# Kernel optimization log

Measured on AMD Instinct MI355X. Metric: run time of the kernel, lower is better.

## Reference

```python
import jax, jax.numpy as jnp
import numpy as np

N_NODES = 50000
N_EDGES = 1600000
IN_DIM = 128
HID = 128
N_GRAPHS = 64
N_CLASSES = 1


def _seg_sum(x, ids, n):
    return jax.ops.segment_sum(x, ids, num_segments=n)


def _gcn_layer(h, W, b, src, dst, src_isqrt, dst_isqrt):
    # DGL GraphConv, norm='both': D_dst^{-1/2} A D_src^{-1/2} (h W) + b
    hw = h @ W                                  # [N, out]
    msg = (hw * src_isqrt[:, None])[src]        # gather -> [E, out]
    agg = _seg_sum(msg, dst, h.shape[0])        # scatter-add -> [N, out]
    return agg * dst_isqrt[:, None] + b


def setup_inputs() -> dict:
    key = jax.random.key(0)
    ks = jax.random.split(key, 16)
    x = jax.random.normal(ks[0], (N_NODES, IN_DIM), dtype=jnp.float32)
    src = jax.random.randint(ks[1], (N_EDGES,), 0, N_NODES)
    dst = jax.random.randint(ks[2], (N_EDGES,), 0, N_NODES)
    graph_id = jnp.sort(jax.random.randint(ks[3], (N_NODES,), 0, N_GRAPHS))
    s = 1.0 / np.sqrt(HID)
    params = {
        'W1': jax.random.uniform(ks[4], (IN_DIM, HID), jnp.float32, -s, s),
        'b1': jnp.zeros((HID,), jnp.float32),
        'W2': jax.random.uniform(ks[5], (HID, HID), jnp.float32, -s, s),
        'b2': jnp.zeros((HID,), jnp.float32),
        'Wc1': jax.random.uniform(ks[6], (HID, HID // 2), jnp.float32, -s, s),
        'bc1': jnp.zeros((HID // 2,), jnp.float32),
        'Wc2': jax.random.uniform(ks[7], (HID // 2, HID // 4), jnp.float32, -s, s),
        'bc2': jnp.zeros((HID // 4,), jnp.float32),
        'Wc3': jax.random.uniform(ks[8], (HID // 4, HID // 8), jnp.float32, -s, s),
        'bc3': jnp.zeros((HID // 8,), jnp.float32),
        'Wc4': jax.random.uniform(ks[9], (HID // 8, N_CLASSES), jnp.float32, -s, s),
        'bc4': jnp.zeros((N_CLASSES,), jnp.float32),
    }
    return dict(x=x, src=src, dst=dst, graph_id=graph_id, num_graphs=N_GRAPHS, **params)


def reference(x, src, dst, graph_id, num_graphs, W1, b1, W2, b2,
              Wc1, bc1, Wc2, bc2, Wc3, bc3, Wc4, bc4):
    n = x.shape[0]
    ones = jnp.ones((src.shape[0],), x.dtype)
    out_deg = jnp.clip(_seg_sum(ones, src, n), 1.0)
    in_deg = jnp.clip(_seg_sum(ones, dst, n), 1.0)
    src_isqrt = jax.lax.rsqrt(out_deg)
    dst_isqrt = jax.lax.rsqrt(in_deg)

    h = jax.nn.relu(_gcn_layer(x, W1, b1, src, dst, src_isqrt, dst_isqrt))
    h = jax.nn.relu(_gcn_layer(h, W2, b2, src, dst, src_isqrt, dst_isqrt))

    # dgl.mean_nodes: per-graph mean of node features
    sums = _seg_sum(h, graph_id, num_graphs)                       # [G, HID]
    cnts = jnp.clip(_seg_sum(jnp.ones((n,), h.dtype), graph_id, num_graphs), 1.0)
    hg = sums / cnts[:, None]

    o = jax.nn.relu(hg @ Wc1 + bc1)
    o = jax.nn.relu(o @ Wc2 + bc2)
    o = jax.nn.relu(o @ Wc3 + bc3)
    return o @ Wc4 + bc4
```

## Files before the change

kernel.cpp:

```cpp
#include <hip/hip_runtime.h>
#include <hip/hip_fp16.h>

#define FDIM 128
#define NGRAPH 64
#define CBLK 256
#define OCH2 12800
#define OSL 64
#define FSTAGE 12288

typedef _Float16 f16;
typedef f16 f16x8 __attribute__((ext_vector_type(8)));
typedef float f32x4 __attribute__((ext_vector_type(4)));
typedef float f32x2 __attribute__((ext_vector_type(2)));

__device__ __forceinline__ int lower_bound_i(const int* a, int n, int v) {
    int lo = 0, hi = n;
    while (lo < hi) { int m = (lo + hi) >> 1; if (a[m] < v) lo = m + 1; else hi = m; }
    return lo;
}

__global__ __launch_bounds__(256) void k_pre(
        const float* __restrict__ W1, f16* __restrict__ W1h, f16* __restrict__ W1l,
        const float* __restrict__ W2, f16* __restrict__ W2h, f16* __restrict__ W2l,
        float* __restrict__ hg, const int* __restrict__ src, const int* __restrict__ dst,
        unsigned* __restrict__ od_part, int* __restrict__ partial,
        int E, int NBIN, int CE4, int NH) {
    __shared__ __align__(16) unsigned shmem_u[OCH2];
    const int t = threadIdx.x;
    int b = blockIdx.x;
    if (b < 128) {
        int i = b * 256 + t;
        if (i < NGRAPH * FDIM) hg[i] = 0.f;
        int j = i & 16383;
        int k = j >> 7, n = j & 127;
        const float* W = (i < 16384) ? W1 : W2;
        f16* Wh = (i < 16384) ? W1h : W2h;
        f16* Wl = (i < 16384) ? W1l : W2l;
        float v = W[j];
        f16 hi = (f16)v;
        Wh[n * FDIM + k] = hi;
        Wl[n * FDIM + k] = (f16)(v - (float)hi);
    } else if (b < 128 + CBLK) {
        b -= 128;
        int* lds = (int*)shmem_u;
        for (int i = t; i < 4 * 257; i += 256) lds[i] = 0;
        __syncthreads();
        const int wv = t >> 6;
        int* hh = &lds[wv * 257];
        const int s = b * CE4, e = min(E, s + CE4);
        for (int i = s + t * 4; i < e; i += 1024) {
            if (i + 4 <= e) {
                uint4 d4 = *(const uint4*)&dst[i];
                atomicAdd(&hh[d4.x >> 8], 1);
                atomicAdd(&hh[d4.y >> 8], 1);
                atomicAdd(&hh[d4.z >> 8], 1);
                atomicAdd(&hh[d4.w >> 8], 1);
            } else {
                for (int j = i; j < e; j++) atomicAdd(&hh[dst[j] >> 8], 1);
            }
        }
        __syncthreads();
        for (int i = t; i < NBIN; i += 256)
            partial[i * CBLK + b] = lds[i] + lds[257 + i] + lds[514 + i] + lds[771 + i];
    } else {
        const int ob = b - 128 - CBLK;
        const int c  = ob >> 6;
        const int sl = ob & (OSL - 1);
        for (int i = t; i < OCH2; i += 256) shmem_u[i] = 0u;
        __syncthreads();
        const int plo = c * OCH2;
        const int vlo = plo * 2;
        const int SE = (((E + OSL - 1) / OSL) + 3) & ~3;
        const int s = sl * SE, e = min(E, s + SE);
        for (int i = s + t * 4; i < e; i += 1024) {
            if (i + 4 <= e) {
                uint4 s4 = *(const uint4*)&src[i];
                int v0 = (int)s4.x - vlo, v1 = (int)s4.y - vlo;
                int v2 = (int)s4.z - vlo, v3 = (int)s4.w - vlo;
                if ((unsigned)v0 < (unsigned)(2 * OCH2))
                    atomicAdd(&shmem_u[v0 >> 1], 1u << ((v0 & 1) * 16));
                if ((unsigned)v1 < (unsigned)(2 * OCH2))
                    atomicAdd(&shmem_u[v1 >> 1], 1u << ((v1 & 1) * 16));
                if ((unsigned)v2 < (unsigned)(2 * OCH2))
                    atomicAdd(&shmem_u[v2 >> 1], 1u << ((v2 & 1) * 16));
                if ((unsigned)v3 < (unsigned)(2 * OCH2))
                    atomicAdd(&shmem_u[v3 >> 1], 1u << ((v3 & 1) * 16));
            } else {
                for (int j = i; j < e; j++) {
                    int v = src[j] - vlo;
                    if ((unsigned)v < (unsigned)(2 * OCH2))
                        atomicAdd(&shmem_u[v >> 1], 1u << ((v & 1) * 16));
                }
            }
        }
        __syncthreads();
        const int hiN = min(NH - plo, OCH2);
        for (int i = t; i < hiN; i += 256)
            od_part[(size_t)sl * NH + plo + i] = shmem_u[i];
    }
}

__global__ __launch_bounds__(256) void k_scan(
        const int* __restrict__ partial, int* __restrict__ offs, int* __restrict__ bsum,
        int M, const unsigned* __restrict__ od_part, float* __restrict__ sisq,
        int NH, int N, int NBIN) {
    __shared__ int lds[256];
    const int t = threadIdx.x;
    int b = blockIdx.x;
    if (b < NBIN) {
        int i = b * 256 + t;
        int v = (i < M) ? partial[i] : 0;
        lds[t] = v;
        __syncthreads();
        for (int off = 1; off < 256; off <<= 1) {
            int x = (t >= off) ? lds[t - off] : 0;
            __syncthreads();
            lds[t] += x;
            __syncthreads();
        }
        if (i < M) offs[i] = lds[t] - v;
        if (t == 255) bsum[b] = lds[t];
    } else {
        b -= NBIN;
        const int i = b * 256 + t;
        if (i < NH) {
            unsigned lo = 0, hi = 0;
#pragma unroll 8
            for (int s = 0; s < OSL; s++) {
                unsigned v = od_part[(size_t)s * NH + i];
                lo += v & 0xFFFFu;
                hi += v >> 16;
            }
            const int n0 = 2 * i, n1 = 2 * i + 1;
            sisq[n0] = rsqrtf((float)max((int)lo, 1));
            if (n1 < N) sisq[n1] = rsqrtf((float)max((int)hi, 1));
        }
    }
}

__global__ __launch_bounds__(256) void k_coarse_scatter(
        const int* __restrict__ src, const int* __restrict__ dst,
        const int* __restrict__ offs, const int* __restrict__ bsum,
        const int* __restrict__ partial,
        unsigned* __restrict__ coarse_buf, int E, int CE4, int NBIN) {
    __shared__ int G[256], lo[256], cur[256], sc[256];
    __shared__ unsigned stage[6272];
    const int t = threadIdx.x, b = blockIdx.x;
    int v = (t < NBIN) ? bsum[t] : 0;
    sc[t] = v;
    __syncthreads();
    for (int off = 1; off < 256; off <<= 1) {
        int x = (t >= off) ? sc[t - off] : 0;
        __syncthreads();
        sc[t] += x;
        __syncthreads();
    }
    if (t < NBIN) G[t] = offs[t * CBLK + b] + (sc[t] - v);
    __syncthreads();
    int hv = (t < NBIN) ? partial[t * CBLK + b] : 0;
    sc[t] = hv;
    __syncthreads();
    for (int off = 1; off < 256; off <<= 1) {
        int x = (t >= off) ? sc[t - off] : 0;
        __syncthreads();
        sc[t] += x;
        __syncthreads();
    }
    lo[t] = sc[t] - hv;
    cur[t] = sc[t] - hv;
    __syncthreads();
    const int s = b * CE4, e = min(E, s + CE4);
    for (int i = s + t * 4; i < e; i += 1024) {
        if (i + 4 <= e) {
            uint4 d4 = *(const uint4*)&dst[i];
            uint4 s4 = *(const uint4*)&src[i];
            int p0 = atomicAdd(&cur[d4.x >> 8], 1);
            int p1 = atomicAdd(&cur[d4.y >> 8], 1);
            int p2 = atomicAdd(&cur[d4.z >> 8], 1);
            int p3 = atomicAdd(&cur[d4.w >> 8], 1);
            stage[p0] = (d4.x << 16) | s4.x;
            stage[p1] = (d4.y << 16) | s4.y;
            stage[p2] = (d4.z << 16) | s4.z;
            stage[p3] = (d4.w << 16) | s4.w;
        } else {
            for (int j = i; j < e; j++) {
                unsigned d = (unsigned)dst[j];
                int p = atomicAdd(&cur[d >> 8], 1);
                stage[p] = (d << 16) | (unsigned)src[j];
            }
        }
    }
    __syncthreads();
    const int nloc = e - s;
    for (int i = t; i < nloc; i += 256) {
        unsigned p = stage[i];
        int f = p >> 24;
        coarse_buf[G[f] + (i - lo[f])] = p;
    }
}

template<bool IN_F16>
__device__ __forceinline__ void gemm_body(
        f16* smem, float* sisql, int blk,
        const void* __restrict__ Xv, const f16* __restrict__ Wh,
        const f16* __restrict__ Wl, const float* __restrict__ sisq,
        unsigned char* __restrict__ out, int N) {
    const int t = threadIdx.x;
    const int w = t >> 6;
    const int lane = t & 63;
    const int base = blk * 128;

    if (t < 128) {
        int row = base + t;
        sisql[t] = (row < N) ? sisq[row] : 1.f;
    }
    for (int i = t; i < 2048; i += 256) {
        int n = i >> 4, kc = (i & 15) * 8;
        *(uint4*)&smem[n * 136 + kc] = *(const uint4*)&Wh[n * FDIM + kc];
    }
    __syncthreads();

    const int mrow = lane & 15;
    const int kq = (lane >> 4) * 8;
    const int arow0 = min(base + w * 32 + mrow, N - 1);
    const int arow1 = min(base + w * 32 + 16 + mrow, N - 1);

    f16x8 a0[4], a1[4];
    if (IN_F16) {
        const f16* X = (const f16*)Xv;
#pragma unroll
        for (int kk = 0; kk < 4; kk++) {
            a0[kk] = *(const f16x8*)&X[(size_t)arow0 * FDIM + kk * 32 + kq];
            a1[kk] = *(const f16x8*)&X[(size_t)arow1 * FDIM + kk * 32 + kq];
        }
    } else {
        const float* X = (const float*)Xv;
#pragma unroll
        for (int kk = 0; kk < 4; kk++) {
            float4 u0 = *(const float4*)&X[(size_t)arow0 * FDIM + kk * 32 + kq];
            float4 u1 = *(const float4*)&X[(size_t)arow0 * FDIM + kk * 32 + kq + 4];
            float4 v0 = *(const float4*)&X[(size_t)arow1 * FDIM + kk * 32 + kq];
            float4 v1 = *(const float4*)&X[(size_t)arow1 * FDIM + kk * 32 + kq + 4];
            f16x8 av;
            av[0] = (f16)u0.x; av[1] = (f16)u0.y; av[2] = (f16)u0.z; av[3] = (f16)u0.w;
            av[4] = (f16)u1.x; av[5] = (f16)u1.y; av[6] = (f16)u1.z; av[7] = (f16)u1.w;
            a0[kk] = av;
            av[0] = (f16)v0.x; av[1] = (f16)v0.y; av[2] = (f16)v0.z; av[3] = (f16)v0.w;
            av[4] = (f16)v1.x; av[5] = (f16)v1.y; av[6] = (f16)v1.z; av[7] = (f16)v1.w;
            a1[kk] = av;
        }
    }

    f32x4 acc0[8], acc1[8];
#pragma unroll
    for (int nt = 0; nt < 8; nt++) {
        acc0[nt] = (f32x4){0.f, 0.f, 0.f, 0.f};
        acc1[nt] = (f32x4){0.f, 0.f, 0.f, 0.f};
    }

#pragma unroll
    for (int kk = 0; kk < 4; kk++) {
#pragma unroll
        for (int nt = 0; nt < 8; nt++) {
            f16x8 bh = *(const f16x8*)&smem[(nt * 16 + mrow) * 136 + kk * 32 + kq];
            f16x8 bl = *(const f16x8*)&Wl[(nt * 16 + mrow) * FDIM + kk * 32 + kq];
            acc0[nt] = __builtin_amdgcn_mfma_f32_16x16x32_f16(a0[kk], bh, acc0[nt], 0, 0, 0);
            acc1[nt] = __builtin_amdgcn_mfma_f32_16x16x32_f16(a1[kk], bh, acc1[nt], 0, 0, 0);
            acc0[nt] = __builtin_amdgcn_mfma_f32_16x16x32_f16(a0[kk], bl, acc0[nt], 0, 0, 0);
            acc1[nt] = __builtin_amdgcn_mfma_f32_16x16x32_f16(a1[kk], bl, acc1[nt], 0, 0, 0);
        }
    }

    const int r0 = (lane >> 4) * 4;
    float sv0[4], sv1[4];
#pragma unroll
    for (int j = 0; j < 4; j++) {
        sv0[j] = sisql[w * 32 + r0 + j];
        sv1[j] = sisql[w * 32 + 16 + r0 + j];
    }
    __syncthreads();
#pragma unroll
    for (int nt = 0; nt < 8; nt++) {
        int c = nt * 16 + mrow;
#pragma unroll
        for (int j = 0; j < 4; j++) {
            smem[(w * 32 + r0 + j) * 136 + c]      = (f16)(acc0[nt][j] * sv0[j]);
            smem[(w * 32 + 16 + r0 + j) * 136 + c] = (f16)(acc1[nt][j] * sv1[j]);
        }
    }
    __syncthreads();
    {
        int r = t >> 1, cb = (t & 1) * 64;
        int row = base + r;
        if (row < N) {
            unsigned char* dstp = out + (size_t)row * FDIM + cb;
#pragma unroll
            for (int g2 = 0; g2 < 4; g2++) {
                unsigned wv[4];
#pragma unroll
                for (int k2 = 0; k2 < 4; k2++) {
                    const f16* p = &smem[r * 136 + cb + g2 * 16 + k2 * 4];
                    int w0 = __builtin_amdgcn_cvt_pk_fp8_f32((float)p[0], (float)p[1], 0, false);
                    w0 = __builtin_amdgcn_cvt_pk_fp8_f32((float)p[2], (float)p[3], w0, true);
                    wv[k2] = (unsigned)w0;
                }
                uint4 u;
                u.x = wv[0]; u.y = wv[1]; u.z = wv[2]; u.w = wv[3];
                *(uint4*)&dstp[g2 * 16] = u;
            }
        }
    }
}

__global__ __launch_bounds__(256) void k_fine_gemm(
        const unsigned* __restrict__ coarse_buf, const int* __restrict__ bsum,
        unsigned short* __restrict__ csr_src, int* __restrict__ row_ptr,
        int N, int E, int NBIN,
        const float* __restrict__ x, const f16* __restrict__ Wh,
        const f16* __restrict__ Wl, const float* __restrict__ sisq,
        unsigned char* __restrict__ hws) {
    __shared__ __align__(16) f16 smem[128 * 136];
    __shared__ float sisql[128];
    const int t = threadIdx.x;
    const int g = blockIdx.x;
    if (g >= NBIN) {
        gemm_body<false>(smem, sisql, g - NBIN, x, Wh, Wl, sisq, hws, N);
        return;
    }
    int* h   = (int*)smem;
    int* sc  = h + 256;
    int* cur = h + 512;
    int* lo  = h + 768;
    unsigned short* stage = (unsigned short*)(h + 1024);
    int bv = (t < NBIN) ? bsum[t] : 0;
    sc[t] = bv;
    __syncthreads();
    for (int off = 1; off < 256; off <<= 1) {
        int xx = (t >= off) ? sc[t - off] : 0;
        __syncthreads();
        sc[t] += xx;
        __syncthreads();
    }
    if (t == 0) { cur[0] = sc[g] - bsum[g]; cur[1] = sc[g]; }
    __syncthreads();
    const int s = cur[0], e = cur[1];
    __syncthreads();
    h[t] = 0;
    __syncthreads();
    for (int i = s + t; i < e; i += 256)
        atomicAdd(&h[(coarse_buf[i] >> 16) & 255], 1);
    __syncthreads();
    int v = h[t];
    sc[t] = v;
    __syncthreads();
    for (int off = 1; off < 256; off <<= 1) {
        int xx = (t >= off) ? sc[t - off] : 0;
        __syncthreads();
        sc[t] += xx;
        __syncthreads();
    }
    const int excl = sc[t] - v;
    const int node = g * 256 + t;
    if (node < N) row_ptr[node] = s + excl;
    if (node == N) row_ptr[N] = s + excl;
    lo[t] = excl;
    cur[t] = excl;
    __syncthreads();
    const int len = e - s;
    if (len <= FSTAGE) {
        for (int i = s + t; i < e; i += 256) {
            unsigned p = coarse_buf[i];
            int f = (p >> 16) & 255;
            int pos = atomicAdd(&cur[f], 1);
            stage[pos] = (unsigned short)(p & 0xFFFFu);
        }
        __syncthreads();
        for (int i = t; i < len; i += 256)
            csr_src[s + i] = stage[i];
    } else {
        for (int i = s + t; i < e; i += 256) {
            unsigned p = coarse_buf[i];
            int f = (p >> 16) & 255;
            int pos = atomicAdd(&cur[f], 1);
            csr_src[s + pos] = (unsigned short)(p & 0xFFFFu);
        }
    }
    if (g == NBIN - 1 && t == 0 && (N & 255) == 0) row_ptr[N] = E;
}

__global__ __launch_bounds__(256) void k_gemm2(
        const f16* __restrict__ X, const f16* __restrict__ Wh,
        const f16* __restrict__ Wl, const float* __restrict__ sisq,
        unsigned char* __restrict__ out, int N) {
    __shared__ __align__(16) f16 smem[128 * 136];
    __shared__ float sisql[128];
    gemm_body<true>(smem, sisql, blockIdx.x, X, Wh, Wl, sisq, out, N);
}

__device__ __forceinline__ void accF8(float* acc, uint2 v) {
    f32x2 a0 = __builtin_amdgcn_cvt_pk_f32_fp8((int)v.x, false);
    f32x2 a1 = __builtin_amdgcn_cvt_pk_f32_fp8((int)v.x, true);
    f32x2 a2 = __builtin_amdgcn_cvt_pk_f32_fp8((int)v.y, false);
    f32x2 a3 = __builtin_amdgcn_cvt_pk_f32_fp8((int)v.y, true);
    acc[0] += a0.x; acc[1] += a0.y; acc[2] += a1.x; acc[3] += a1.y;
    acc[4] += a2.x; acc[5] += a2.y; acc[6] += a3.x; acc[7] += a3.y;
}

template<bool POOL>
__global__ __launch_bounds__(256) void k_aggregate(
        const unsigned char* __restrict__ hws,
        const unsigned short* __restrict__ csr_src,
        const int* __restrict__ row_ptr,
        const float* __restrict__ bias, f16* __restrict__ out,
        const int* __restrict__ gid, float* __restrict__ hg, int N) {
    const int t = threadIdx.x;
    const int node = blockIdx.x * 8 + (t >> 5);
    const int ln = t & 31;
    const int half = ln >> 4;
    const int fbase = (ln & 15) * 8;

    int s = 0, e = 0;
    if (node < N) { s = row_ptr[node]; e = row_ptr[node + 1]; }
    const int len = e - s;
    const int mid = s + ((len + 1) >> 1);
    int i  = half ? mid : s;
    const int en = half ? e : mid;

    float acc[8];
#pragma unroll
    for (int j = 0; j < 8; j++) acc[j] = 0.f;

    for (; i + 8 <= en; i += 8) {
        int u[8];
#pragma unroll
        for (int j = 0; j < 8; j++) u[j] = csr_src[i + j];
        uint2 v[8];
#pragma unroll
        for (int j = 0; j < 8; j++)
            v[j] = *(const uint2*)(hws + (size_t)u[j] * FDIM + fbase);
#pragma unroll
        for (int j = 0; j < 8; j++) accF8(acc, v[j]);
    }
    if (i + 4 <= en) {
        int u[4];
#pragma unroll
        for (int j = 0; j < 4; j++) u[j] = csr_src[i + j];
        uint2 v[4];
#pragma unroll
        for (int j = 0; j < 4; j++)
            v[j] = *(const uint2*)(hws + (size_t)u[j] * FDIM + fbase);
#pragma unroll
        for (int j = 0; j < 4; j++) accF8(acc, v[j]);
        i += 4;
    }
    for (; i < en; i++) {
        int u = csr_src[i];
        uint2 v = *(const uint2*)(hws + (size_t)u * FDIM + fbase);
        accF8(acc, v);
    }

#pragma unroll
    for (int j = 0; j < 8; j++) acc[j] += __shfl_xor(acc[j], 16, 64);

    const float d = rsqrtf((float)max(len, 1));
    float res[8];
#pragma unroll
    for (int j = 0; j < 8; j++)
        res[j] = fmaxf(fmaf(acc[j], d, bias[fbase + j]), 0.f);

    if (!POOL) {
        if (node < N && half == 0) {
            f16 r16[8];
#pragma unroll
            for (int j = 0; j < 8; j++) r16[j] = (f16)res[j];
            *(uint4*)(out + (size_t)node * FDIM + fbase) = *(const uint4*)r16;
        }
    } else {
        __shared__ float hgl[8 * 128];
        const int nfirst = blockIdx.x * 8;
        const int nlast = min(nfirst + 7, N - 1);
        const int g0 = gid[nfirst];
        const int span = gid[nlast] - g0 + 1;
        if (span <= 8) {
            for (int k = t; k < span * 128; k += 256) hgl[k] = 0.f;
            __syncthreads();
            if (node < N && half == 0) {
                const int gg = gid[node] - g0;
#pragma unroll
                for (int j = 0; j < 8; j++)
                    atomicAdd(&hgl[gg * 128 + fbase + j], res[j]);
            }
            __syncthreads();
            for (int k = t; k < span * 128; k += 256)
                atomicAdd(&hg[g0 * 128 + k], hgl[k]);
        } else {
            if (node < N && half == 0) {
                const int gg = gid[node];
#pragma unroll
                for (int j = 0; j < 8; j++)
                    atomicAdd(&hg[gg * 128 + fbase + j], res[j]);
            }
        }
    }
}

__global__ __launch_bounds__(256) void k_mlp(
        const float* __restrict__ hg, const int* __restrict__ gid, int N,
        const float* __restrict__ Wc1, const float* __restrict__ bc1,
        const float* __restrict__ Wc2, const float* __restrict__ bc2,
        const float* __restrict__ Wc3, const float* __restrict__ bc3,
        const float* __restrict__ Wc4, const float* __restrict__ bc4,
        float* __restrict__ out) {
    __shared__ float A[NGRAPH * 128];
    __shared__ float O1[NGRAPH * 64];
    __shared__ float O2[NGRAPH * 32];
    __shared__ float O3[NGRAPH * 16];
    __shared__ float inv_cnt[NGRAPH];
    const int t = threadIdx.x;

    if (t < NGRAPH) {
        int s = lower_bound_i(gid, N, t);
        int e = lower_bound_i(gid, N, t + 1);
        inv_cnt[t] = 1.f / fmaxf((float)(e - s), 1.f);
    }
    __syncthreads();

    for (int i = t; i < NGRAPH * 128; i += 256) A[i] = hg[i] * inv_cnt[i >> 7];
    __syncthreads();

    for (int i = t; i < NGRAPH * 64; i += 256) {
        int g = i >> 6, o = i & 63;
        float a = bc1[o];
        for (int k = 0; k < 128; k++) a = fmaf(A[g * 128 + k], Wc1[k * 64 + o], a);
        O1[i] = fmaxf(a, 0.f);
    }
    __syncthreads();

    for (int i = t; i < NGRAPH * 32; i += 256) {
        int g = i >> 5, o = i & 31;
        float a = bc2[o];
        for (int k = 0; k < 64; k++) a = fmaf(O1[g * 64 + k], Wc2[k * 32 + o], a);
        O2[i] = fmaxf(a, 0.f);
    }
    __syncthreads();

    for (int i = t; i < NGRAPH * 16; i += 256) {
        int g = i >> 4, o = i & 15;
        float a = bc3[o];
        for (int k = 0; k < 32; k++) a = fmaf(O2[g * 32 + k], Wc3[k * 16 + o], a);
        O3[i] = fmaxf(a, 0.f);
    }
    __syncthreads();

    if (t < NGRAPH) {
        float a = bc4[0];
        for (int k = 0; k < 16; k++) a = fmaf(O3[t * 16 + k], Wc4[k], a);
        out[t] = a;
    }
}

extern "C" void kernel_launch(void* const* d_in, const int* in_sizes, int n_in,
                              void* d_out, int out_size, void* d_ws, size_t ws_size,
                              hipStream_t stream) {
    const float* x   = (const float*)d_in[0];
    const int*   src = (const int*)d_in[1];
    const int*   dst = (const int*)d_in[2];
    const int*   gid = (const int*)d_in[3];
    const float* W1  = (const float*)d_in[5];
    const float* b1  = (const float*)d_in[6];
    const float* W2  = (const float*)d_in[7];
    const float* b2  = (const float*)d_in[8];
    const float* Wc1 = (const float*)d_in[9];
    const float* bc1 = (const float*)d_in[10];
    const float* Wc2 = (const float*)d_in[11];
    const float* bc2 = (const float*)d_in[12];
    const float* Wc3 = (const float*)d_in[13];
    const float* bc3 = (const float*)d_in[14];
    const float* Wc4 = (const float*)d_in[15];
    const float* bc4 = (const float*)d_in[16];
    float* out = (float*)d_out;

    const int N = in_sizes[0] / FDIM;
    const int E = in_sizes[1];

    const int NBIN = (N + 255) >> 8;
    const int M    = NBIN * CBLK;
    const int CE4  = (((E + CBLK - 1) / CBLK) + 3) & ~3;
    const int NH   = (N + 1) >> 1;
    const int OC2  = (NH + OCH2 - 1) / OCH2;
    const int MB   = (NH + 255) >> 8;

    char* w = (char*)d_ws;
    size_t off = 0;
    auto alloc = [&](size_t bytes) -> void* {
        void* p = w + off;
        off = (off + bytes + 255) & ~(size_t)255;
        return p;
    };
    unsigned char* hws = (unsigned char*)alloc((size_t)N * FDIM);
    f16*   h       = (f16*)   alloc((size_t)N * FDIM * 2);
    unsigned short* csr_src = (unsigned short*)alloc((size_t)E * 2);
    unsigned* coarse_buf = (unsigned*)alloc((size_t)E * 4);
    unsigned* od_part = (unsigned*)alloc((size_t)OSL * NH * 4);
    int*   partial = (int*)   alloc((size_t)M * 4);
    int*   offs    = (int*)   alloc((size_t)M * 4);
    int*   row_ptr = (int*)   alloc((size_t)(N + 1) * 4);
    float* sisq    = (float*) alloc((size_t)N * 4);
    int*   bsum    = (int*)   alloc(256 * 4);
    float* hg      = (float*) alloc(NGRAPH * FDIM * 4);
    f16*   W1t     = (f16*)   alloc(FDIM * FDIM * 2);
    f16*   W1l     = (f16*)   alloc(FDIM * FDIM * 2);
    f16*   W2t     = (f16*)   alloc(FDIM * FDIM * 2);
    f16*   W2l     = (f16*)   alloc(FDIM * FDIM * 2);

    const int gT = (N + 127) / 128;
    const int gA = (N + 7) / 8;

    k_pre<<<128 + CBLK + OC2 * OSL, 256, 0, stream>>>(
        W1, W1t, W1l, W2, W2t, W2l, hg, src, dst, od_part, partial, E, NBIN, CE4, NH);
    k_scan<<<NBIN + MB, 256, 0, stream>>>(partial, offs, bsum, M, od_part, sisq, NH, N, NBIN);
    k_coarse_scatter<<<CBLK, 256, 0, stream>>>(
        src, dst, offs, bsum, partial, coarse_buf, E, CE4, NBIN);
    k_fine_gemm<<<NBIN + gT, 256, 0, stream>>>(
        coarse_buf, bsum, csr_src, row_ptr, N, E, NBIN,
        x, W1t, W1l, sisq, hws);
    k_aggregate<false><<<gA, 256, 0, stream>>>(hws, csr_src, row_ptr, b1, h, nullptr, nullptr, N);
    k_gemm2<<<gT, 256, 0, stream>>>(h, W2t, W2l, sisq, hws, N);
    k_aggregate<true><<<gA, 256, 0, stream>>>(hws, csr_src, row_ptr, b2, nullptr, gid, hg, N);
    k_mlp<<<1, 256, 0, stream>>>(hg, gid, N, Wc1, bc1, Wc2, bc2, Wc3, bc3, Wc4, bc4, out);
}
```

Measured before the change: 277.6 us.

## Fuse layer-1 aggregation with layer-2 GEMM through shared memory

Merges the first aggregation kernel and the second GEMM into one kernel. Each block gathers and sums neighbor features for 128 nodes into an LDS tile, then runs the MFMA GEMM directly from that tile. This removes the fp16 h buffer round trip through global memory and one launch. In exchange, 128-node blocks do the gather in 8 serial rounds of 16 nodes with one 16-lane group per node, which gives fewer blocks and less latency hiding for the irregular gathers. A separate output buffer avoids overwriting hws while other blocks still read it.

```diff
diff --git a/kernel.cpp b/kernel.cpp
--- a/kernel.cpp
+++ b/kernel.cpp
@@ -388,15 +388,6 @@
     if (g == NBIN - 1 && t == 0 && (N & 255) == 0) row_ptr[N] = E;
 }
 
-__global__ __launch_bounds__(256) void k_gemm2(
-        const f16* __restrict__ X, const f16* __restrict__ Wh,
-        const f16* __restrict__ Wl, const float* __restrict__ sisq,
-        unsigned char* __restrict__ out, int N) {
-    __shared__ __align__(16) f16 smem[128 * 136];
-    __shared__ float sisql[128];
-    gemm_body<true>(smem, sisql, blockIdx.x, X, Wh, Wl, sisq, out, N);
-}
-
 __device__ __forceinline__ void accF8(float* acc, uint2 v) {
     f32x2 a0 = __builtin_amdgcn_cvt_pk_f32_fp8((int)v.x, false);
     f32x2 a1 = __builtin_amdgcn_cvt_pk_f32_fp8((int)v.x, true);
@@ -406,12 +397,148 @@
     acc[4] += a2.x; acc[5] += a2.y; acc[6] += a3.x; acc[7] += a3.y;
 }
 
-template<bool POOL>
-__global__ __launch_bounds__(256) void k_aggregate(
+__global__ __launch_bounds__(256) void k_agg_gemm2(
         const unsigned char* __restrict__ hws,
         const unsigned short* __restrict__ csr_src,
         const int* __restrict__ row_ptr,
-        const float* __restrict__ bias, f16* __restrict__ out,
+        const float* __restrict__ bias,
+        const f16* __restrict__ Wh,
+        const f16* __restrict__ Wl,
+        const float* __restrict__ sisq,
+        unsigned char* __restrict__ out, int N) {
+    __shared__ __align__(16) f16 smem[128 * 136];
+    __shared__ float sisql[128];
+    const int t = threadIdx.x;
+    const int base = blockIdx.x * 128;
+    if (t < 128) {
+        int row = base + t;
+        sisql[t] = (row < N) ? sisq[row] : 1.f;
+    }
+    const int grp = t >> 4;
+    const int l = t & 15;
+    const int fbase = l * 8;
+    for (int k = 0; k < 8; k++) {
+        const int nl = k * 16 + grp;
+        const int node = base + nl;
+        int s = 0, e = 0;
+        if (node < N) { s = row_ptr[node]; e = row_ptr[node + 1]; }
+        float acc[8];
+#pragma unroll
+        for (int j = 0; j < 8; j++) acc[j] = 0.f;
+        int i = s;
+        for (; i + 8 <= e; i += 8) {
+            int u[8];
+#pragma unroll
+            for (int j = 0; j < 8; j++) u[j] = csr_src[i + j];
+            uint2 v[8];
+#pragma unroll
+            for (int j = 0; j < 8; j++)
+                v[j] = *(const uint2*)(hws + (size_t)u[j] * FDIM + fbase);
+#pragma unroll
+            for (int j = 0; j < 8; j++) accF8(acc, v[j]);
+        }
+        if (i + 4 <= e) {
+            int u[4];
+#pragma unroll
+            for (int j = 0; j < 4; j++) u[j] = csr_src[i + j];
+            uint2 v[4];
+#pragma unroll
+            for (int j = 0; j < 4; j++)
+                v[j] = *(const uint2*)(hws + (size_t)u[j] * FDIM + fbase);
+#pragma unroll
+            for (int j = 0; j < 4; j++) accF8(acc, v[j]);
+            i += 4;
+        }
+        for (; i < e; i++) {
+            int u = csr_src[i];
+            uint2 v = *(const uint2*)(hws + (size_t)u * FDIM + fbase);
+            accF8(acc, v);
+        }
+        const float d = rsqrtf((float)max(e - s, 1));
+        f16 r16[8];
+#pragma unroll
+        for (int j = 0; j < 8; j++)
+            r16[j] = (f16)fmaxf(fmaf(acc[j], d, bias[fbase + j]), 0.f);
+        *(uint4*)&smem[nl * 136 + fbase] = *(const uint4*)r16;
+    }
+    __syncthreads();
+
+    const int w = t >> 6;
+    const int lane = t & 63;
+    const int mrow = lane & 15;
+    const int kq = (lane >> 4) * 8;
+    const int ar0 = w * 32 + mrow;
+    const int ar1 = w * 32 + 16 + mrow;
+    f16x8 a0[4], a1[4];
+#pragma unroll
+    for (int kk = 0; kk < 4; kk++) {
+        a0[kk] = *(const f16x8*)&smem[ar0 * 136 + kk * 32 + kq];
+        a1[kk] = *(const f16x8*)&smem[ar1 * 136 + kk * 32 + kq];
+    }
+    f32x4 acc0[8], acc1[8];
+#pragma unroll
+    for (int nt = 0; nt < 8; nt++) {
+        acc0[nt] = (f32x4){0.f, 0.f, 0.f, 0.f};
+        acc1[nt] = (f32x4){0.f, 0.f, 0.f, 0.f};
+    }
+#pragma unroll
+    for (int kk = 0; kk < 4; kk++) {
+#pragma unroll
+        for (int nt = 0; nt < 8; nt++) {
+            f16x8 bh = *(const f16x8*)&Wh[(nt * 16 + mrow) * FDIM + kk * 32 + kq];
+            f16x8 bl = *(const f16x8*)&Wl[(nt * 16 + mrow) * FDIM + kk * 32 + kq];
+            acc0[nt] = __builtin_amdgcn_mfma_f32_16x16x32_f16(a0[kk], bh, acc0[nt], 0, 0, 0);
+            acc1[nt] = __builtin_amdgcn_mfma_f32_16x16x32_f16(a1[kk], bh, acc1[nt], 0, 0, 0);
+            acc0[nt] = __builtin_amdgcn_mfma_f32_16x16x32_f16(a0[kk], bl, acc0[nt], 0, 0, 0);
+            acc1[nt] = __builtin_amdgcn_mfma_f32_16x16x32_f16(a1[kk], bl, acc1[nt], 0, 0, 0);
+        }
+    }
+    const int r0 = (lane >> 4) * 4;
+    float sv0[4], sv1[4];
+#pragma unroll
+    for (int j = 0; j < 4; j++) {
+        sv0[j] = sisql[w * 32 + r0 + j];
+        sv1[j] = sisql[w * 32 + 16 + r0 + j];
+    }
+    __syncthreads();
+#pragma unroll
+    for (int nt = 0; nt < 8; nt++) {
+        int c = nt * 16 + mrow;
+#pragma unroll
+        for (int j = 0; j < 4; j++) {
+            smem[(w * 32 + r0 + j) * 136 + c]      = (f16)(acc0[nt][j] * sv0[j]);
+            smem[(w * 32 + 16 + r0 + j) * 136 + c] = (f16)(acc1[nt][j] * sv1[j]);
+        }
+    }
+    __syncthreads();
+    {
+        int r = t >> 1, cb = (t & 1) * 64;
+        int row = base + r;
+        if (row < N) {
+            unsigned char* dstp = out + (size_t)row * FDIM + cb;
+#pragma unroll
+            for (int g2 = 0; g2 < 4; g2++) {
+                unsigned wv[4];
+#pragma unroll
+                for (int k2 = 0; k2 < 4; k2++) {
+                    const f16* p = &smem[r * 136 + cb + g2 * 16 + k2 * 4];
+                    int w0 = __builtin_amdgcn_cvt_pk_fp8_f32((float)p[0], (float)p[1], 0, false);
+                    w0 = __builtin_amdgcn_cvt_pk_fp8_f32((float)p[2], (float)p[3], w0, true);
+                    wv[k2] = (unsigned)w0;
+                }
+                uint4 u;
+                u.x = wv[0]; u.y = wv[1]; u.z = wv[2]; u.w = wv[3];
+                *(uint4*)&dstp[g2 * 16] = u;
+            }
+        }
+    }
+}
+
+__global__ __launch_bounds__(256) void k_aggregate_pool(
+        const unsigned char* __restrict__ hws,
+        const unsigned short* __restrict__ csr_src,
+        const int* __restrict__ row_ptr,
+        const float* __restrict__ bias,
         const int* __restrict__ gid, float* __restrict__ hg, int N) {
     const int t = threadIdx.x;
     const int node = blockIdx.x * 8 + (t >> 5);
@@ -468,38 +595,29 @@
     for (int j = 0; j < 8; j++)
         res[j] = fmaxf(fmaf(acc[j], d, bias[fbase + j]), 0.f);
 
-    if (!POOL) {
+    __shared__ float hgl[8 * 128];
+    const int nfirst = blockIdx.x * 8;
+    const int nlast = min(nfirst + 7, N - 1);
+    const int g0 = gid[nfirst];
+    const int span = gid[nlast] - g0 + 1;
+    if (span <= 8) {
+        for (int k = t; k < span * 128; k += 256) hgl[k] = 0.f;
+        __syncthreads();
         if (node < N && half == 0) {
-            f16 r16[8];
-#pragma unroll
-            for (int j = 0; j < 8; j++) r16[j] = (f16)res[j];
-            *(uint4*)(out + (size_t)node * FDIM + fbase) = *(const uint4*)r16;
-        }
+            const int gg = gid[node] - g0;
+#pragma unroll
+            for (int j = 0; j < 8; j++)
+                atomicAdd(&hgl[gg * 128 + fbase + j], res[j]);
+        }
+        __syncthreads();
+        for (int k = t; k < span * 128; k += 256)
+            atomicAdd(&hg[g0 * 128 + k], hgl[k]);
     } else {
-        __shared__ float hgl[8 * 128];
-        const int nfirst = blockIdx.x * 8;
-        const int nlast = min(nfirst + 7, N - 1);
-        const int g0 = gid[nfirst];
-        const int span = gid[nlast] - g0 + 1;
-        if (span <= 8) {
-            for (int k = t; k < span * 128; k += 256) hgl[k] = 0.f;
-            __syncthreads();
-            if (node < N && half == 0) {
-                const int gg = gid[node] - g0;
-#pragma unroll
-                for (int j = 0; j < 8; j++)
-                    atomicAdd(&hgl[gg * 128 + fbase + j], res[j]);
-            }
-            __syncthreads();
-            for (int k = t; k < span * 128; k += 256)
-                atomicAdd(&hg[g0 * 128 + k], hgl[k]);
-        } else {
-            if (node < N && half == 0) {
-                const int gg = gid[node];
-#pragma unroll
-                for (int j = 0; j < 8; j++)
-                    atomicAdd(&hg[gg * 128 + fbase + j], res[j]);
-            }
+        if (node < N && half == 0) {
+            const int gg = gid[node];
+#pragma unroll
+            for (int j = 0; j < 8; j++)
+                atomicAdd(&hg[gg * 128 + fbase + j], res[j]);
         }
     }
 }
@@ -597,8 +715,8 @@
         off = (off + bytes + 255) & ~(size_t)255;
         return p;
     };
-    unsigned char* hws = (unsigned char*)alloc((size_t)N * FDIM);
-    f16*   h       = (f16*)   alloc((size_t)N * FDIM * 2);
+    unsigned char* hws  = (unsigned char*)alloc((size_t)N * FDIM);
+    unsigned char* hws2 = (unsigned char*)alloc((size_t)N * FDIM);
     unsigned short* csr_src = (unsigned short*)alloc((size_t)E * 2);
     unsigned* coarse_buf = (unsigned*)alloc((size_t)E * 4);
     unsigned* od_part = (unsigned*)alloc((size_t)OSL * NH * 4);
@@ -624,8 +742,8 @@
     k_fine_gemm<<<NBIN + gT, 256, 0, stream>>>(
         coarse_buf, bsum, csr_src, row_ptr, N, E, NBIN,
         x, W1t, W1l, sisq, hws);
-    k_aggregate<false><<<gA, 256, 0, stream>>>(hws, csr_src, row_ptr, b1, h, nullptr, nullptr, N);
-    k_gemm2<<<gT, 256, 0, stream>>>(h, W2t, W2l, sisq, hws, N);
-    k_aggregate<true><<<gA, 256, 0, stream>>>(hws, csr_src, row_ptr, b2, nullptr, gid, hg, N);
+    k_agg_gemm2<<<gT, 256, 0, stream>>>(
+        hws, csr_src, row_ptr, b1, W2t, W2l, sisq, hws2, N);
+    k_aggregate_pool<<<gA, 256, 0, stream>>>(hws2, csr_src, row_ptr, b2, gid, hg, N);
     k_mlp<<<1, 256, 0, stream>>>(hg, gid, N, Wc1, bc1, Wc2, bc2, Wc3, bc3, Wc4, bc4, out);
 }
```

New measurement: 301.5 us. 8.6% more time.
